# Kernel tuning notes

Measured on AMD Instinct MI355X. Metric: run time of the kernel, lower is better.

Reference implementation:

```python
import jax, jax.numpy as jnp
import numpy as np

NPOINT = 2048
RADII = (0.4, 0.8)
NSAMPLES = (16, 32)
EPS = 1e-5


def _fps(xyz, npoint):
    # iterative farthest point sampling, start at index 0 (matches CUDA kernel)
    B, N, _ = xyz.shape

    def step(carry, _):
        dist, last = carry  # dist [B,N], last [B]
        lx = jnp.take_along_axis(xyz, last[:, None, None], axis=1)  # [B,1,3]
        d = jnp.sum((xyz - lx) ** 2, axis=-1)  # [B,N]
        dist = jnp.minimum(dist, d)
        nxt = jnp.argmax(dist, axis=1).astype(jnp.int32)
        return (dist, nxt), last

    init = (jnp.full((B, N), 1e10, xyz.dtype), jnp.zeros((B,), jnp.int32))
    _, idxs = jax.lax.scan(step, init, None, length=npoint)
    return idxs.T  # [B, npoint]


def _ball_query(radius, nsample, xyz, new_xyz):
    # first-nsample points within radius, in original order; pad with first hit (0 if none)
    N = xyz.shape[1]
    d2 = jnp.sum((new_xyz[:, :, None, :] - xyz[:, None, :, :]) ** 2, axis=-1)  # [B,S,N]
    mask = d2 < radius * radius
    ar = jnp.arange(N, dtype=jnp.int32)
    key = jnp.where(mask, ar, N + ar)  # in-range first, stable original order
    order = jnp.argsort(key, axis=-1)[..., :nsample].astype(jnp.int32)  # [B,S,ns]
    cnt = mask.sum(axis=-1, keepdims=True)  # [B,S,1]
    valid = jnp.arange(nsample) < cnt
    return jnp.where(valid, order, order[..., :1])


def _bn_relu(x):
    # training-mode BatchNorm (gamma=1, beta=0) over all dims but channel (last)
    red = tuple(range(x.ndim - 1))
    mu = x.mean(axis=red, keepdims=True)
    var = x.var(axis=red, keepdims=True)
    return jax.nn.relu((x - mu) * jax.lax.rsqrt(var + EPS))


def _scale(xyz, new_xyz, feats, radius, nsample, ws):
    idx = _ball_query(radius, nsample, xyz, new_xyz)  # [B,S,ns]
    B, S, ns = idx.shape
    flat = idx.reshape(B, S * ns)
    gx = jnp.take_along_axis(xyz, flat[..., None], axis=1).reshape(B, S, ns, 3)
    gx = gx - new_xyz[:, :, None, :]  # relative coords
    gf = jnp.take_along_axis(feats, flat[..., None], axis=1).reshape(B, S, ns, -1)
    h = jnp.concatenate([gx, gf], axis=-1)  # [B,S,ns,3+C]
    for w in ws:
        h = _bn_relu(h @ w)  # pointwise conv (kernel 1) + BN + ReLU
    return h.max(axis=2)  # max-pool over group -> [B,S,Cout]


def setup_inputs() -> dict:
    key = jax.random.key(0)
    ks = jax.random.split(key, 16)
    s = 0.02
    return {
        "xyz": jax.random.normal(ks[0], (8, 8192, 3), jnp.float32),
        "features": jax.random.normal(ks[1], (8, 8192, 64), jnp.float32),
        "w0_0": jax.random.normal(ks[2], (67, 64), jnp.float32) * s,
        "w0_1": jax.random.normal(ks[3], (64, 64), jnp.float32) * s,
        "w0_2": jax.random.normal(ks[4], (64, 128), jnp.float32) * s,
        "w1_0": jax.random.normal(ks[5], (67, 64), jnp.float32) * s,
        "w1_1": jax.random.normal(ks[6], (64, 64), jnp.float32) * s,
        "w1_2": jax.random.normal(ks[7], (64, 128), jnp.float32) * s,
        "agg_w": jax.random.normal(ks[8], (256, 256), jnp.float32) * s,
        "agg_b": jax.random.normal(ks[9], (256,), jnp.float32) * s,
        "conf_w": jax.random.normal(ks[10], (256, 256), jnp.float32) * s,
        "cls_w": jax.random.normal(ks[11], (256, 3), jnp.float32) * s,
        "cls_b": jax.random.normal(ks[12], (3,), jnp.float32) * s,
    }


def reference(xyz, features, w0_0, w0_1, w0_2, w1_0, w1_1, w1_2,
              agg_w, agg_b, conf_w, cls_w, cls_b):
    idx = _fps(xyz, NPOINT)  # [B,S]
    new_xyz = jnp.take_along_axis(xyz, idx[..., None], axis=1)  # [B,S,3]
    f0 = _scale(xyz, new_xyz, features, RADII[0], NSAMPLES[0], (w0_0, w0_1, w0_2))
    f1 = _scale(xyz, new_xyz, features, RADII[1], NSAMPLES[1], (w1_0, w1_1, w1_2))
    h = jnp.concatenate([f0, f1], axis=-1)  # [B,S,256]
    h = _bn_relu(h @ agg_w + agg_b)  # aggregation Linear + BN + ReLU
    c = _bn_relu(h @ conf_w)  # confidence hidden layer
    cls = c @ cls_w + cls_b  # [B,S,num_class]
    return new_xyz, h, cls
```

## Files before the change

kernel.cpp:

```cpp
#include <hip/hip_runtime.h>
#include <cstdint>
#include <cstddef>

constexpr int Bb = 8;
constexpr int Nn = 8192;
constexpr int Ss = 2048;
constexpr int BS = Bb * Ss;

typedef float vfloat2 __attribute__((ext_vector_type(2)));

__global__ __launch_bounds__(1024) void fps_kernel(const float* __restrict__ xyz,
                                                   float* __restrict__ new_xyz) {
  __shared__ float lx[Nn * 3];
  __shared__ int sidx[Ss];
  __shared__ unsigned long long slotV[2];
  __shared__ int slotI[2];
  const int b = blockIdx.x;
  const int tid = threadIdx.x;
  const float* xb = xyz + (size_t)b * Nn * 3;
  for (int e = tid; e < Nn * 3; e += 1024) lx[e] = xb[e];
  if (tid == 0) {
    slotV[0] = 0ull; slotV[1] = 0ull;
    slotI[0] = 0x7fffffff; slotI[1] = 0x7fffffff;
  }
  __syncthreads();

  vfloat2 px2[4], py2[4], pz2[4], df2[4];
  double dist[8];
#pragma unroll
  for (int jj = 0; jj < 4; ++jj) {
    const int p0 = tid + (2 * jj) * 1024, p1 = tid + (2 * jj + 1) * 1024;
    px2[jj] = (vfloat2){lx[p0 * 3 + 0], lx[p1 * 3 + 0]};
    py2[jj] = (vfloat2){lx[p0 * 3 + 1], lx[p1 * 3 + 1]};
    pz2[jj] = (vfloat2){lx[p0 * 3 + 2], lx[p1 * 3 + 2]};
    df2[jj] = (vfloat2){3.0e38f, 3.0e38f};
    dist[2 * jj] = 1e10;
    dist[2 * jj + 1] = 1e10;
  }
  const int lane = tid & 63;
  int cur = 0;
  double lv = 0.0;
  int li = 0x7fffffff;
  double wv_c = 0.0;
  for (int i = 0; i < Ss; ++i) {
    if (tid == 0) sidx[i] = cur;
    const float cxf = lx[cur * 3 + 0], cyf = lx[cur * 3 + 1], czf = lx[cur * 3 + 2];
    const vfloat2 cx2 = {cxf, cxf}, cy2 = {cyf, cyf}, cz2 = {czf, czf};
    unsigned need = 0;
#pragma unroll
    for (int jj = 0; jj < 4; ++jj) {
      const vfloat2 dx = px2[jj] - cx2;
      const vfloat2 dy = py2[jj] - cy2;
      const vfloat2 dz = pz2[jj] - cz2;
      const vfloat2 d2 = dx * dx + dy * dy + dz * dz;
      need |= (d2.x <= df2[jj].x) ? (1u << (2 * jj)) : 0u;
      need |= (d2.y <= df2[jj].y) ? (1u << (2 * jj + 1)) : 0u;
    }
    bool changed = false;
    if (need) {
#pragma unroll
      for (int j = 0; j < 8; ++j) {
        if (need & (1u << j)) {
          const float pxs = px2[j >> 1][j & 1];
          const float pys = py2[j >> 1][j & 1];
          const float pzs = pz2[j >> 1][j & 1];
          double dx = __dsub_rn((double)pxs, (double)cxf);
          double dy = __dsub_rn((double)pys, (double)cyf);
          double dz = __dsub_rn((double)pzs, (double)czf);
          double d = __dadd_rn(__dadd_rn(__dmul_rn(dx, dx), __dmul_rn(dy, dy)),
                               __dmul_rn(dz, dz));
          if (d < dist[j]) {
            dist[j] = d;
            const float dfn = (float)d * 1.000002f;
            if (j & 1) df2[j >> 1].y = dfn; else df2[j >> 1].x = dfn;
            changed = true;
          }
        }
      }
    }
    const unsigned long long anyb = __ballot(changed);
    if (changed) {
      lv = -1.0;
      li = 0;
#pragma unroll
      for (int j = 0; j < 8; ++j) {
        if (dist[j] > lv) { lv = dist[j]; li = tid + j * 1024; }
      }
    }
    if (anyb) {
      double bv = lv;
#pragma unroll
      for (int off = 1; off < 64; off <<= 1) bv = fmax(bv, __shfl_xor(bv, off));
      wv_c = bv;
    }
    const int pb = i & 1;
    if (lane == 0) atomicMax(&slotV[pb], __double_as_longlong(wv_c));
    __syncthreads();
    const double W = __longlong_as_double((long long)slotV[pb]);
    if (lv == W) atomicMin(&slotI[pb], li);
    if (tid == 0) {
      slotV[pb ^ 1] = 0ull;
      slotI[pb ^ 1] = 0x7fffffff;
    }
    __syncthreads();
    cur = slotI[pb];
  }
  __syncthreads();
  float* nxb = new_xyz + (size_t)b * Ss * 3;
  for (int e = tid; e < Ss * 3; e += 1024) {
    const int i = e / 3, c = e - i * 3;
    nxb[e] = lx[sidx[i] * 3 + c];
  }
}

__global__ __launch_bounds__(256) void ballq_kernel(const float* __restrict__ xyz,
                                                    const float* __restrict__ nxyz,
                                                    int* __restrict__ idx0,
                                                    int* __restrict__ idx1) {
  const int wid = threadIdx.x >> 6, lane = threadIdx.x & 63;
  const int bs = blockIdx.x * 4 + wid;
  const int b = bs >> 11;
  const float* xb = xyz + (size_t)b * Nn * 3;
  const double cx = (double)nxyz[bs * 3 + 0];
  const double cy = (double)nxyz[bs * 3 + 1];
  const double cz = (double)nxyz[bs * 3 + 2];
  const double R0 = 0.4 * 0.4, R1 = 0.8 * 0.8;
  int cnt0 = 0, cnt1 = 0, first0 = 0, first1 = 0;
  const unsigned long long lmask = (1ull << lane) - 1ull;
  for (int base = 0; base < Nn; base += 64) {
    const int p = base + lane;
    double dx = __dsub_rn((double)xb[p * 3 + 0], cx);
    double dy = __dsub_rn((double)xb[p * 3 + 1], cy);
    double dz = __dsub_rn((double)xb[p * 3 + 2], cz);
    double d2 = __dadd_rn(__dadd_rn(__dmul_rn(dx, dx), __dmul_rn(dy, dy)), __dmul_rn(dz, dz));
    const bool in0 = d2 < R0, in1 = d2 < R1;
    unsigned long long m0 = __ballot(in0);
    unsigned long long m1 = __ballot(in1);
    if (cnt0 < 16 && m0) {
      if (cnt0 == 0) first0 = base + __builtin_ctzll(m0);
      int r = (int)__popcll(m0 & lmask);
      if (in0 && cnt0 + r < 16) idx0[bs * 16 + cnt0 + r] = p;
      cnt0 += (int)__popcll(m0);
    }
    if (cnt1 < 32 && m1) {
      if (cnt1 == 0) first1 = base + __builtin_ctzll(m1);
      int r = (int)__popcll(m1 & lmask);
      if (in1 && cnt1 + r < 32) idx1[bs * 32 + cnt1 + r] = p;
      cnt1 += (int)__popcll(m1);
    }
    if (cnt0 >= 16 && cnt1 >= 32) break;
  }
  const int f0 = cnt0 < 16 ? cnt0 : 16;
  for (int j = f0 + lane; j < 16; j += 64) idx0[bs * 16 + j] = first0;
  const int f1 = cnt1 < 32 ? cnt1 : 32;
  for (int j = f1 + lane; j < 32; j += 64) idx1[bs * 32 + j] = first1;
}

template <int COUT, int KTOT, int MODE, int NS, bool POOL, bool BIAS>
__global__ __launch_bounds__(256) void mlp_gemm(
    const float* __restrict__ xin, const float* __restrict__ xin2,
    const float* __restrict__ bnp, const float* __restrict__ bnp2,
    const float* __restrict__ w, const float* __restrict__ bias,
    const int* __restrict__ gidx, const float* __restrict__ xyz,
    const float* __restrict__ nxyz, const float* __restrict__ feats,
    float* __restrict__ out, float* __restrict__ P) {
  constexpr int KC = (KTOT <= 68) ? KTOT : 32;
  constexpr int NCH = (KTOT + KC - 1) / KC;
  constexpr int TC = COUT / 16;
  constexpr int XPAD = KC + 1;
  constexpr int XSZ = 64 * XPAD;
  constexpr int EPI = (POOL ? 48 : 32) * COUT;
  constexpr int SM = (XSZ + KC * COUT > EPI) ? (XSZ + KC * COUT) : EPI;
  __shared__ float smem[SM];
  float* xS = smem;
  float* wS = smem + XSZ;

  const int tid = threadIdx.x;
  const int cg = tid & 15, rg = tid >> 4;
  const int row0 = blockIdx.x * 64;
  float acc[4][TC];
#pragma unroll
  for (int i = 0; i < 4; ++i)
#pragma unroll
    for (int t = 0; t < TC; ++t) acc[i][t] = 0.f;

  for (int ch = 0; ch < NCH; ++ch) {
    const int k0 = ch * KC;
    if (ch) __syncthreads();
    for (int e = tid; e < 64 * KC; e += 256) {
      const int r = e / KC, kk = e - r * KC;
      const int kg = k0 + kk;
      const int rowg = row0 + r;
      float v;
      if constexpr (MODE == 0) {
        const int bs = rowg / NS;
        const int p = gidx[rowg];
        const int bb = bs >> 11;
        if (kg < 3)
          v = xyz[(bb * Nn + p) * 3 + kg] - nxyz[bs * 3 + kg];
        else
          v = feats[((bb * Nn + p) << 6) + (kg - 3)];
      } else if constexpr (MODE == 1) {
        v = fmaxf((xin[(size_t)rowg * 64 + kg] - bnp[kg]) * bnp[64 + kg], 0.f);
      } else if constexpr (MODE == 2) {
        if (kg < 128)
          v = fmaxf((xin[(size_t)rowg * 128 + kg] - bnp[kg]) * bnp[128 + kg], 0.f);
        else {
          const int k2 = kg - 128;
          v = fmaxf((xin2[(size_t)rowg * 128 + k2] - bnp2[k2]) * bnp2[128 + k2], 0.f);
        }
      } else {
        v = xin[(size_t)rowg * 256 + kg];
      }
      xS[r * XPAD + kk] = v;
    }
    for (int e = tid; e < KC * COUT; e += 256) {
      const int kk = e / COUT, c = e - kk * COUT;
      wS[kk * COUT + c] = w[(size_t)(k0 + kk) * COUT + c];
    }
    __syncthreads();
    for (int kk = 0; kk < KC; ++kk) {
      float xr[4];
#pragma unroll
      for (int i = 0; i < 4; ++i) xr[i] = xS[(rg * 4 + i) * XPAD + kk];
#pragma unroll
      for (int t = 0; t < TC; t += 4) {
        const float4 wv = *(const float4*)&wS[kk * COUT + cg * TC + t];
#pragma unroll
        for (int i = 0; i < 4; ++i) {
          acc[i][t + 0] = fmaf(xr[i], wv.x, acc[i][t + 0]);
          acc[i][t + 1] = fmaf(xr[i], wv.y, acc[i][t + 1]);
          acc[i][t + 2] = fmaf(xr[i], wv.z, acc[i][t + 2]);
          acc[i][t + 3] = fmaf(xr[i], wv.w, acc[i][t + 3]);
        }
      }
    }
  }
  __syncthreads();
  if constexpr (BIAS) {
#pragma unroll
    for (int t = 0; t < TC; ++t) {
      const float bv = bias[cg * TC + t];
#pragma unroll
      for (int i = 0; i < 4; ++i) acc[i][t] += bv;
    }
  }
  float* ssum = smem;
  float* ssq = smem + 16 * COUT;
  float* pbuf = smem + 32 * COUT;
  const int colb = cg * TC;
#pragma unroll
  for (int t = 0; t < TC; ++t) {
    float s = 0.f, q = 0.f, m = -3.4e38f;
#pragma unroll
    for (int i = 0; i < 4; ++i) {
      const float v = acc[i][t];
      s += v;
      q = fmaf(v, v, q);
      m = fmaxf(m, v);
    }
    ssum[rg * COUT + colb + t] = s;
    ssq[rg * COUT + colb + t] = q;
    if constexpr (POOL) pbuf[rg * COUT + colb + t] = m;
  }
  __syncthreads();
  const int gX = gridDim.x;
  for (int c = tid; c < COUT; c += 256) {
    float s = 0.f, q = 0.f;
#pragma unroll
    for (int rr = 0; rr < 16; ++rr) {
      s += ssum[rr * COUT + c];
      q += ssq[rr * COUT + c];
    }
    P[(size_t)c * gX + blockIdx.x] = s;
    P[(size_t)(COUT + c) * gX + blockIdx.x] = q;
  }
  if constexpr (POOL) {
    constexpr int G = 64 / NS, RPG = NS / 4;
    for (int o = tid; o < G * COUT; o += 256) {
      const int g = o / COUT, c = o - g * COUT;
      float m = pbuf[(g * RPG) * COUT + c];
#pragma unroll
      for (int qq = 1; qq < RPG; ++qq) m = fmaxf(m, pbuf[(g * RPG + qq) * COUT + c]);
      out[(size_t)(blockIdx.x * G + g) * COUT + c] = m;
    }
  } else {
#pragma unroll
    for (int i = 0; i < 4; ++i) {
      float* op = out + (size_t)(row0 + rg * 4 + i) * COUT + colb;
#pragma unroll
      for (int t = 0; t < TC; t += 4) {
        *(float4*)(op + t) = make_float4(acc[i][t], acc[i][t + 1], acc[i][t + 2], acc[i][t + 3]);
      }
    }
  }
}

__global__ __launch_bounds__(256) void bn_finalize(const float* __restrict__ P, int gX,
                                                   int M, int C, float* __restrict__ bnp) {
  __shared__ double sh[512];
  const int c = blockIdx.x;
  const int tid = threadIdx.x;
  const float* psum = P + (size_t)c * gX;
  const float* psq = P + (size_t)(C + c) * gX;
  double s = 0, q = 0;
  for (int i = tid; i < gX; i += 256) {
    s += (double)psum[i];
    q += (double)psq[i];
  }
  sh[tid] = s;
  sh[256 + tid] = q;
  __syncthreads();
  for (int off = 128; off; off >>= 1) {
    if (tid < off) {
      sh[tid] += sh[tid + off];
      sh[256 + tid] += sh[256 + tid + off];
    }
    __syncthreads();
  }
  if (tid == 0) {
    const double invM = 1.0 / (double)M;
    const double mu = sh[0] * invM;
    const double var = sh[256] * invM - mu * mu;
    bnp[c] = (float)mu;
    bnp[C + c] = (float)(1.0 / sqrt(var + 1e-5));
  }
}

__global__ __launch_bounds__(256) void h_store_kernel(const float* __restrict__ agg,
                                                      const float* __restrict__ bnp,
                                                      float* __restrict__ hout) {
  const int t = blockIdx.x * 256 + threadIdx.x;
  const int c = t & 255;
  const float v = (agg[t] - bnp[c]) * bnp[256 + c];
  hout[t] = fmaxf(v, 0.f);
}

__global__ __launch_bounds__(256) void cls_kernel(const float* __restrict__ craw,
                                                  const float* __restrict__ bnp,
                                                  const float* __restrict__ clsw,
                                                  const float* __restrict__ clsb,
                                                  float* __restrict__ outc) {
  const int wid = threadIdx.x >> 6, lane = threadIdx.x & 63;
  const int row = blockIdx.x * 4 + wid;
  const float* cr = craw + (size_t)row * 256;
  float a0 = 0.f, a1 = 0.f, a2 = 0.f;
#pragma unroll 4
  for (int k = lane; k < 256; k += 64) {
    float x = fmaxf((cr[k] - bnp[k]) * bnp[256 + k], 0.f);
    a0 = fmaf(x, clsw[k * 3 + 0], a0);
    a1 = fmaf(x, clsw[k * 3 + 1], a1);
    a2 = fmaf(x, clsw[k * 3 + 2], a2);
  }
#pragma unroll
  for (int off = 32; off; off >>= 1) {
    a0 += __shfl_down(a0, off);
    a1 += __shfl_down(a1, off);
    a2 += __shfl_down(a2, off);
  }
  if (lane == 0) {
    outc[row * 3 + 0] = a0 + clsb[0];
    outc[row * 3 + 1] = a1 + clsb[1];
    outc[row * 3 + 2] = a2 + clsb[2];
  }
}

extern "C" void kernel_launch(void* const* d_in, const int* in_sizes, int n_in,
                              void* d_out, int out_size, void* d_ws, size_t ws_size,
                              hipStream_t stream) {
  (void)in_sizes; (void)n_in; (void)out_size; (void)ws_size;
  const float* xyz = (const float*)d_in[0];
  const float* feats = (const float*)d_in[1];
  const float* w00 = (const float*)d_in[2];
  const float* w01 = (const float*)d_in[3];
  const float* w02 = (const float*)d_in[4];
  const float* w10 = (const float*)d_in[5];
  const float* w11 = (const float*)d_in[6];
  const float* w12 = (const float*)d_in[7];
  const float* aggw = (const float*)d_in[8];
  const float* aggb = (const float*)d_in[9];
  const float* confw = (const float*)d_in[10];
  const float* clsw = (const float*)d_in[11];
  const float* clsb = (const float*)d_in[12];

  float* outp = (float*)d_out;
  float* nxyz = outp;
  float* hout = outp + (size_t)BS * 3;
  float* clsout = hout + (size_t)BS * 256;

  char* ws = (char*)d_ws;
  const size_t MB = 1u << 20;
  int* idx0 = (int*)(ws + 0);
  int* idx1 = (int*)(ws + 1 * MB);
  float* bnb = (float*)(ws + 3 * MB);
  float* P = (float*)(ws + 4 * MB);
  float* pool0 = (float*)(ws + 12 * MB);
  float* pool1 = (float*)(ws + 20 * MB);
  float* aggraw = (float*)(ws + 28 * MB);
  float* confraw = (float*)(ws + 44 * MB);
  float* hA = (float*)(ws + 60 * MB);

  fps_kernel<<<Bb, 1024, 0, stream>>>(xyz, nxyz);
  ballq_kernel<<<BS / 4, 256, 0, stream>>>(xyz, nxyz, idx0, idx1);

  mlp_gemm<64, 67, 0, 16, false, false><<<4096, 256, 0, stream>>>(
      nullptr, nullptr, nullptr, nullptr, w00, nullptr, idx0, xyz, nxyz, feats, hA, P);
  bn_finalize<<<64, 256, 0, stream>>>(P, 4096, 262144, 64, bnb + 0);
  mlp_gemm<64, 64, 1, 1, false, false><<<4096, 256, 0, stream>>>(
      hA, nullptr, bnb + 0, nullptr, w01, nullptr, nullptr, nullptr, nullptr, nullptr, hA, P);
  bn_finalize<<<64, 256, 0, stream>>>(P, 4096, 262144, 64, bnb + 128);
  mlp_gemm<128, 64, 1, 16, true, false><<<4096, 256, 0, stream>>>(
      hA, nullptr, bnb + 128, nullptr, w02, nullptr, nullptr, nullptr, nullptr, nullptr, pool0, P);
  bn_finalize<<<128, 256, 0, stream>>>(P, 4096, 262144, 128, bnb + 256);

  mlp_gemm<64, 67, 0, 32, false, false><<<8192, 256, 0, stream>>>(
      nullptr, nullptr, nullptr, nullptr, w10, nullptr, idx1, xyz, nxyz, feats, hA, P);
  bn_finalize<<<64, 256, 0, stream>>>(P, 8192, 524288, 64, bnb + 512);
  mlp_gemm<64, 64, 1, 1, false, false><<<8192, 256, 0, stream>>>(
      hA, nullptr, bnb + 512, nullptr, w11, nullptr, nullptr, nullptr, nullptr, nullptr, hA, P);
  bn_finalize<<<64, 256, 0, stream>>>(P, 8192, 524288, 64, bnb + 640);
  mlp_gemm<128, 64, 1, 32, true, false><<<8192, 256, 0, stream>>>(
      hA, nullptr, bnb + 640, nullptr, w12, nullptr, nullptr, nullptr, nullptr, nullptr, pool1, P);
  bn_finalize<<<128, 256, 0, stream>>>(P, 8192, 524288, 128, bnb + 768);

  mlp_gemm<256, 256, 2, 1, false, true><<<256, 256, 0, stream>>>(
      pool0, pool1, bnb + 256, bnb + 768, aggw, aggb, nullptr, nullptr, nullptr, nullptr, aggraw, P);
  bn_finalize<<<256, 256, 0, stream>>>(P, 256, 16384, 256, bnb + 1024);
  h_store_kernel<<<BS, 256, 0, stream>>>(aggraw, bnb + 1024, hout);

  mlp_gemm<256, 256, 3, 1, false, false><<<256, 256, 0, stream>>>(
      hout, nullptr, nullptr, nullptr, confw, nullptr, nullptr, nullptr, nullptr, nullptr, confraw, P);
  bn_finalize<<<256, 256, 0, stream>>>(P, 256, 16384, 256, bnb + 1536);

  cls_kernel<<<BS / 4, 256, 0, stream>>>(confraw, bnb + 1536, clsw, clsb, clsout);
}
```

Before: 3.855 ms.

## Skip FPS per-point checks via lane min/max bound; fuse h BN into conf GEMM

In FPS, each thread now takes the minimum of its 8 float distances and compares it against the largest float threshold it holds. If nothing can shrink it skips the per-point double-precision path, and it recomputes that threshold only when its distances change. The wave reduction moves from double to float shuffles, and only lanes holding the wave max perform the double atomicMax. Separately, the h BN+ReLU store kernel is removed: the conf GEMM (new MODE 4) applies the normalisation while loading its input and writes h as a side output. The float-only wave reduction risks ties or rounding differences when selecting the argmax, and every thread matching the wave max now issues an atomic.

After: 3.762 ms. 1.02x faster.

```diff
diff --git a/kernel.cpp b/kernel.cpp
--- a/kernel.cpp
+++ b/kernel.cpp
@@ -37,30 +37,33 @@
     dist[2 * jj] = 1e10;
     dist[2 * jj + 1] = 1e10;
   }
-  const int lane = tid & 63;
+  float lmax = 3.0e38f;
   int cur = 0;
-  double lv = 0.0;
+  double lv = -1.0;
   int li = 0x7fffffff;
-  double wv_c = 0.0;
+  float lv32 = -1.0f;
+  float wv32_c = -1.0f;
   for (int i = 0; i < Ss; ++i) {
     if (tid == 0) sidx[i] = cur;
     const float cxf = lx[cur * 3 + 0], cyf = lx[cur * 3 + 1], czf = lx[cur * 3 + 2];
     const vfloat2 cx2 = {cxf, cxf}, cy2 = {cyf, cyf}, cz2 = {czf, czf};
-    unsigned need = 0;
+    vfloat2 d2v[4];
 #pragma unroll
     for (int jj = 0; jj < 4; ++jj) {
       const vfloat2 dx = px2[jj] - cx2;
       const vfloat2 dy = py2[jj] - cy2;
       const vfloat2 dz = pz2[jj] - cz2;
-      const vfloat2 d2 = dx * dx + dy * dy + dz * dz;
-      need |= (d2.x <= df2[jj].x) ? (1u << (2 * jj)) : 0u;
-      need |= (d2.y <= df2[jj].y) ? (1u << (2 * jj + 1)) : 0u;
-    }
+      d2v[jj] = dx * dx + dy * dy + dz * dz;
+    }
+    const float dmin = fminf(fminf(fminf(d2v[0].x, d2v[0].y), fminf(d2v[1].x, d2v[1].y)),
+                             fminf(fminf(d2v[2].x, d2v[2].y), fminf(d2v[3].x, d2v[3].y)));
     bool changed = false;
-    if (need) {
+    if (dmin <= lmax) {
 #pragma unroll
       for (int j = 0; j < 8; ++j) {
-        if (need & (1u << j)) {
+        const float d2s = d2v[j >> 1][j & 1];
+        const float dfs = (j & 1) ? df2[j >> 1].y : df2[j >> 1].x;
+        if (d2s <= dfs) {
           const float pxs = px2[j >> 1][j & 1];
           const float pys = py2[j >> 1][j & 1];
           const float pzs = pz2[j >> 1][j & 1];
@@ -77,24 +80,27 @@
           }
         }
       }
+      if (changed) {
+        lv = -1.0;
+        li = 0;
+#pragma unroll
+        for (int j = 0; j < 8; ++j) {
+          if (dist[j] > lv) { lv = dist[j]; li = tid + j * 1024; }
+        }
+        lv32 = (float)lv;
+        lmax = fmaxf(fmaxf(fmaxf(df2[0].x, df2[0].y), fmaxf(df2[1].x, df2[1].y)),
+                     fmaxf(fmaxf(df2[2].x, df2[2].y), fmaxf(df2[3].x, df2[3].y)));
+      }
     }
     const unsigned long long anyb = __ballot(changed);
-    if (changed) {
-      lv = -1.0;
-      li = 0;
-#pragma unroll
-      for (int j = 0; j < 8; ++j) {
-        if (dist[j] > lv) { lv = dist[j]; li = tid + j * 1024; }
-      }
-    }
     if (anyb) {
-      double bv = lv;
-#pragma unroll
-      for (int off = 1; off < 64; off <<= 1) bv = fmax(bv, __shfl_xor(bv, off));
-      wv_c = bv;
+      float m32 = lv32;
+#pragma unroll
+      for (int off = 1; off < 64; off <<= 1) m32 = fmaxf(m32, __shfl_xor(m32, off));
+      wv32_c = m32;
     }
     const int pb = i & 1;
-    if (lane == 0) atomicMax(&slotV[pb], __double_as_longlong(wv_c));
+    if (lv32 == wv32_c) atomicMax(&slotV[pb], (unsigned long long)__double_as_longlong(lv));
     __syncthreads();
     const double W = __longlong_as_double((long long)slotV[pb]);
     if (lv == W) atomicMin(&slotI[pb], li);
@@ -163,7 +169,7 @@
     const float* __restrict__ w, const float* __restrict__ bias,
     const int* __restrict__ gidx, const float* __restrict__ xyz,
     const float* __restrict__ nxyz, const float* __restrict__ feats,
-    float* __restrict__ out, float* __restrict__ P) {
+    float* __restrict__ hw, float* __restrict__ out, float* __restrict__ P) {
   constexpr int KC = (KTOT <= 68) ? KTOT : 32;
   constexpr int NCH = (KTOT + KC - 1) / KC;
   constexpr int TC = COUT / 16;
@@ -210,7 +216,8 @@
           v = fmaxf((xin2[(size_t)rowg * 128 + k2] - bnp2[k2]) * bnp2[128 + k2], 0.f);
         }
       } else {
-        v = xin[(size_t)rowg * 256 + kg];
+        v = fmaxf((xin[(size_t)rowg * 256 + kg] - bnp[kg]) * bnp[256 + kg], 0.f);
+        hw[(size_t)rowg * 256 + kg] = v;
       }
       xS[r * XPAD + kk] = v;
     }
@@ -325,15 +332,6 @@
     bnp[c] = (float)mu;
     bnp[C + c] = (float)(1.0 / sqrt(var + 1e-5));
   }
-}
-
-__global__ __launch_bounds__(256) void h_store_kernel(const float* __restrict__ agg,
-                                                      const float* __restrict__ bnp,
-                                                      float* __restrict__ hout) {
-  const int t = blockIdx.x * 256 + threadIdx.x;
-  const int c = t & 255;
-  const float v = (agg[t] - bnp[c]) * bnp[256 + c];
-  hout[t] = fmaxf(v, 0.f);
 }
 
 __global__ __launch_bounds__(256) void cls_kernel(const float* __restrict__ craw,
@@ -404,32 +402,31 @@
   ballq_kernel<<<BS / 4, 256, 0, stream>>>(xyz, nxyz, idx0, idx1);
 
   mlp_gemm<64, 67, 0, 16, false, false><<<4096, 256, 0, stream>>>(
-      nullptr, nullptr, nullptr, nullptr, w00, nullptr, idx0, xyz, nxyz, feats, hA, P);
+      nullptr, nullptr, nullptr, nullptr, w00, nullptr, idx0, xyz, nxyz, feats, nullptr, hA, P);
   bn_finalize<<<64, 256, 0, stream>>>(P, 4096, 262144, 64, bnb + 0);
   mlp_gemm<64, 64, 1, 1, false, false><<<4096, 256, 0, stream>>>(
-      hA, nullptr, bnb + 0, nullptr, w01, nullptr, nullptr, nullptr, nullptr, nullptr, hA, P);
+      hA, nullptr, bnb + 0, nullptr, w01, nullptr, nullptr, nullptr, nullptr, nullptr, nullptr, hA, P);
   bn_finalize<<<64, 256, 0, stream>>>(P, 4096, 262144, 64, bnb + 128);
   mlp_gemm<128, 64, 1, 16, true, false><<<4096, 256, 0, stream>>>(
-      hA, nullptr, bnb + 128, nullptr, w02, nullptr, nullptr, nullptr, nullptr, nullptr, pool0, P);
+      hA, nullptr, bnb + 128, nullptr, w02, nullptr, nullptr, nullptr, nullptr, nullptr, nullptr, pool0, P);
   bn_finalize<<<128, 256, 0, stream>>>(P, 4096, 262144, 128, bnb + 256);
 
   mlp_gemm<64, 67, 0, 32, false, false><<<8192, 256, 0, stream>>>(
-      nullptr, nullptr, nullptr, nullptr, w10, nullptr, idx1, xyz, nxyz, feats, hA, P);
+      nullptr, nullptr, nullptr, nullptr, w10, nullptr, idx1, xyz, nxyz, feats, nullptr, hA, P);
   bn_finalize<<<64, 256, 0, stream>>>(P, 8192, 524288, 64, bnb + 512);
   mlp_gemm<64, 64, 1, 1, false, false><<<8192, 256, 0, stream>>>(
-      hA, nullptr, bnb + 512, nullptr, w11, nullptr, nullptr, nullptr, nullptr, nullptr, hA, P);
+      hA, nullptr, bnb + 512, nullptr, w11, nullptr, nullptr, nullptr, nullptr, nullptr, nullptr, hA, P);
   bn_finalize<<<64, 256, 0, stream>>>(P, 8192, 524288, 64, bnb + 640);
   mlp_gemm<128, 64, 1, 32, true, false><<<8192, 256, 0, stream>>>(
-      hA, nullptr, bnb + 640, nullptr, w12, nullptr, nullptr, nullptr, nullptr, nullptr, pool1, P);
+      hA, nullptr, bnb + 640, nullptr, w12, nullptr, nullptr, nullptr, nullptr, nullptr, nullptr, pool1, P);
   bn_finalize<<<128, 256, 0, stream>>>(P, 8192, 524288, 128, bnb + 768);
 
   mlp_gemm<256, 256, 2, 1, false, true><<<256, 256, 0, stream>>>(
-      pool0, pool1, bnb + 256, bnb + 768, aggw, aggb, nullptr, nullptr, nullptr, nullptr, aggraw, P);
+      pool0, pool1, bnb + 256, bnb + 768, aggw, aggb, nullptr, nullptr, nullptr, nullptr, nullptr, aggraw, P);
   bn_finalize<<<256, 256, 0, stream>>>(P, 256, 16384, 256, bnb + 1024);
-  h_store_kernel<<<BS, 256, 0, stream>>>(aggraw, bnb + 1024, hout);
-
-  mlp_gemm<256, 256, 3, 1, false, false><<<256, 256, 0, stream>>>(
-      hout, nullptr, nullptr, nullptr, confw, nullptr, nullptr, nullptr, nullptr, nullptr, confraw, P);
+
+  mlp_gemm<256, 256, 4, 1, false, false><<<256, 256, 0, stream>>>(
+      aggraw, nullptr, bnb + 1024, nullptr, confw, nullptr, nullptr, nullptr, nullptr, nullptr, hout, confraw, P);
   bn_finalize<<<256, 256, 0, stream>>>(P, 256, 16384, 256, bnb + 1536);
 
   cls_kernel<<<BS / 4, 256, 0, stream>>>(confraw, bnb + 1536, clsw, clsb, clsout);
```
